# Optimization experiments

Measured on AMD Instinct MI355X. Metric: run time of the kernel, lower is better.

Reference implementation:

```python
import jax, jax.numpy as jnp
import numpy as np

N_HEAD = 12


def setup_inputs() -> dict:
    key = jax.random.key(0)
    ks = jax.random.split(key, 6)
    B, T, C = 8, 1024, 768
    x = jax.random.normal(ks[0], (B, T, C), dtype=jnp.float32)
    w_attn = jax.random.normal(ks[1], (C, 3 * C), dtype=jnp.float32) * 0.02
    b_attn = jnp.zeros((3 * C,), dtype=jnp.float32)
    w_proj = jax.random.normal(ks[2], (C, C), dtype=jnp.float32) * 0.02
    b_proj = jnp.zeros((C,), dtype=jnp.float32)
    rel_emb = jax.random.normal(ks[3], (2 * 1024 - 1, C // N_HEAD), dtype=jnp.float32) * 0.02
    return {"x": x, "w_attn": w_attn, "b_attn": b_attn,
            "w_proj": w_proj, "b_proj": b_proj, "rel_emb": rel_emb}


def reference(x, w_attn, b_attn, w_proj, b_proj, rel_emb):
    b, t, c = x.shape
    h = N_HEAD
    d = c // h
    scale = d ** -0.5
    # fused QKV projection
    qkv = x @ w_attn + b_attn                       # [b, t, 3c]
    q, k, v = jnp.split(qkv, 3, axis=-1)
    split_heads = lambda z: z.reshape(b, t, h, d).transpose(0, 2, 1, 3)  # [b,h,t,d]
    q, k, v = map(split_heads, (q, k, v))
    q = q * scale
    # content scores
    scores = jnp.einsum('bhid,bhjd->bhij', q, k)    # [b,h,t,t]
    # relative position bias: embed lookup + rel-shift (zero row prepended, last dropped)
    rel = rel_emb[:t]                               # [t, d]
    rel = jnp.concatenate([jnp.zeros_like(rel[:1]), rel], axis=0)[:-1]
    scores = scores + jnp.einsum('bhid,jd->bhij', q, rel)
    # causal mask
    causal = jnp.tril(jnp.ones((t, t), dtype=bool))
    scores = jnp.where(causal, scores, -jnp.inf)
    probs = jax.nn.softmax(scores, axis=-1)
    y = jnp.einsum('bhij,bhjd->bhid', probs, v)     # [b,h,t,d]
    y = y.transpose(0, 2, 1, 3).reshape(b, t, c)
    return y @ w_proj + b_proj
```

## Files before the change

### kernel.cpp

```cpp
#include <hip/hip_runtime.h>
#include <stdint.h>


typedef __attribute__((ext_vector_type(8))) short short8;
typedef __attribute__((ext_vector_type(4))) float f32x4;
typedef __attribute__((ext_vector_type(4))) unsigned short ushort4v;

#define DEV static __device__ __forceinline__

DEV float bf2f(unsigned short u) {
    union { unsigned int u; float f; } v; v.u = ((unsigned int)u) << 16; return v.f;
}
DEV unsigned short f2bf(float f) {
    union { float f; unsigned int u; } v; v.f = f;
    unsigned int u = v.u;
    return (unsigned short)((u + 0x7fffu + ((u >> 16) & 1u)) >> 16);
}

typedef const __attribute__((address_space(1))) void* gas_ptr;
typedef __attribute__((address_space(3))) void* las_ptr;
DEV void glds16(const void* g, void* l) {
    __builtin_amdgcn_global_load_lds((gas_ptr)g, (las_ptr)l, 16, 0, 0);
}

__global__ void detect_dtype(const unsigned int* __restrict__ w, int* __restrict__ flag) {
    __shared__ int cnt;
    if (threadIdx.x == 0) cnt = 0;
    __syncthreads();
    int c = 0;
    for (int i = threadIdx.x; i < 8192; i += 256) {
        unsigned int b1 = (w[i] >> 8) & 0x7F;
        c += (b1 >= 0x38 && b1 <= 0x3E) ? 1 : 0;
    }
    atomicAdd(&cnt, c);
    __syncthreads();
    if (threadIdx.x == 0) *flag = (cnt > 4096) ? 1 : 0;
}

__global__ __launch_bounds__(256) void cast_x(
    const void* __restrict__ x, unsigned short* __restrict__ xo,
    const int* __restrict__ flag)
{
    int i = (blockIdx.x * 256 + threadIdx.x) * 4;
    if (*flag) {
        *(ushort4v*)(xo + i) = *(const ushort4v*)((const unsigned short*)x + i);
    } else {
        f32x4 v = *(const f32x4*)((const float*)x + i);
        ushort4v o;
#pragma unroll
        for (int j = 0; j < 4; ++j) o[j] = f2bf(v[j]);
        *(ushort4v*)(xo + i) = o;
    }
}

__global__ __launch_bounds__(256) void cast_small(
    const void* __restrict__ rel, const void* __restrict__ ba, const void* __restrict__ bp,
    unsigned short* __restrict__ rel_o, unsigned short* __restrict__ ba_o,
    unsigned short* __restrict__ bp_o, const int* __restrict__ flag)
{
    int i = blockIdx.x * 256 + threadIdx.x;
    if (i >= 134080) return;
    int isbf = *flag;
    const void* src; unsigned short* dst; int off;
    if (i < 131008)      { src = rel; dst = rel_o; off = i; }
    else if (i < 133312) { src = ba;  dst = ba_o;  off = i - 131008; }
    else                 { src = bp;  dst = bp_o;  off = i - 133312; }
    dst[off] = isbf ? ((const unsigned short*)src)[off]
                    : f2bf(((const float*)src)[off]);
}

__global__ __launch_bounds__(256) void transpose_w(
    const void* __restrict__ in, unsigned short* __restrict__ out,
    int R, int C, const int* __restrict__ flag)
{
    __shared__ unsigned short tile[64][66];
    const int t = threadIdx.x;
    const int cb = blockIdx.x * 64;
    const int rb = blockIdx.y * 64;
    if (*flag) {
        const unsigned short* inp = (const unsigned short*)in;
        const int c8 = (t & 7) * 8;
        const int r = t >> 3;
#pragma unroll
        for (int p = 0; p < 2; ++p) {
            int rr = r + p * 32;
            short8 v = *(const short8*)(inp + (size_t)(rb + rr) * C + cb + c8);
#pragma unroll
            for (int i = 0; i < 8; ++i) tile[rr][c8 + i] = (unsigned short)v[i];
        }
    } else {
        const float* inp = (const float*)in;
        const int c4 = (t & 15) * 4;
        const int r = t >> 4;
#pragma unroll
        for (int p = 0; p < 4; ++p) {
            int rr = r + p * 16;
            f32x4 v = *(const f32x4*)(inp + (size_t)(rb + rr) * C + cb + c4);
#pragma unroll
            for (int i = 0; i < 4; ++i) tile[rr][c4 + i] = f2bf(v[i]);
        }
    }
    __syncthreads();
    {
        const int c8 = (t & 7) * 8;
        const int r = t >> 3;
#pragma unroll
        for (int p = 0; p < 2; ++p) {
            int oc = r + p * 32;
            short8 v;
#pragma unroll
            for (int i = 0; i < 8; ++i) v[i] = (short)tile[c8 + i][oc];
            *(short8*)(out + (size_t)(cb + oc) * R + rb + c8) = v;
        }
    }
}

#define GEMM_PROLOG(A_, Bt_)                                                     \
    __shared__ __align__(16) unsigned short Abuf[128 * 32];                      \
    __shared__ __align__(16) unsigned short Bbuf[128 * 32];                      \
    const int t = threadIdx.x;                                                   \
    const int wave = t >> 6, lane = t & 63;                                      \
    const int lo = lane & 15, hi = lane >> 4;                                    \
    const int wr = wave >> 1, wc = wave & 1;                                     \
    const int bm = blockIdx.x * 128;                                             \
    const int bn = blockIdx.y * 128;                                             \
    int L0 = t << 4, L1 = (t + 256) << 4;                                        \
    int S0 = L0 ^ (((L0 >> 7) & 3) << 4);                                        \
    int S1 = L1 ^ (((L1 >> 7) & 3) << 4);                                        \
    int r0 = S0 >> 6, o0 = (S0 & 63) >> 1;                                       \
    int r1 = S1 >> 6, o1 = (S1 & 63) >> 1;                                       \
    const unsigned short* Ab = (A_) + (size_t)bm * 768;                          \
    const unsigned short* Bb = (Bt_) + (size_t)bn * 768;                         \
    char* lA0 = (char*)Abuf + ((wave * 64) << 4);                                \
    char* lA1 = (char*)Abuf + ((256 + wave * 64) << 4);                          \
    char* lB0 = (char*)Bbuf + ((wave * 64) << 4);                                \
    char* lB1 = (char*)Bbuf + ((256 + wave * 64) << 4);                          \
    const char* ap[4]; const char* bp_[4];                                       \
    _Pragma("unroll")                                                            \
    for (int m = 0; m < 4; ++m) {                                                \
        int Pa = ((wr * 64 + m * 16 + lo) << 6) + (hi << 4);                     \
        ap[m] = (const char*)Abuf + (Pa ^ (((Pa >> 7) & 3) << 4));               \
        int Pb = ((wc * 64 + m * 16 + lo) << 6) + (hi << 4);                     \
        bp_[m] = (const char*)Bbuf + (Pb ^ (((Pb >> 7) & 3) << 4));              \
    }                                                                            \
    f32x4 acc[4][4];                                                             \
    _Pragma("unroll")                                                            \
    for (int m = 0; m < 4; ++m)                                                  \
        _Pragma("unroll")                                                        \
        for (int n = 0; n < 4; ++n) acc[m][n] = (f32x4){0.f, 0.f, 0.f, 0.f};     \
    for (int k0 = 0; k0 < 768; k0 += 32) {                                       \
        glds16(Ab + (size_t)r0 * 768 + k0 + o0, lA0);                            \
        glds16(Ab + (size_t)r1 * 768 + k0 + o1, lA1);                            \
        glds16(Bb + (size_t)r0 * 768 + k0 + o0, lB0);                            \
        glds16(Bb + (size_t)r1 * 768 + k0 + o1, lB1);                            \
        __syncthreads();                                                         \
        short8 af[4], bfv[4];                                                    \
        _Pragma("unroll")                                                        \
        for (int m = 0; m < 4; ++m) af[m] = *(const short8*)ap[m];               \
        _Pragma("unroll")                                                        \
        for (int n = 0; n < 4; ++n) bfv[n] = *(const short8*)bp_[n];             \
        _Pragma("unroll")                                                        \
        for (int m = 0; m < 4; ++m)                                              \
            _Pragma("unroll")                                                    \
            for (int n = 0; n < 4; ++n)                                          \
                acc[m][n] = __builtin_amdgcn_mfma_f32_16x16x32_bf16(             \
                    af[m], bfv[n], acc[m][n], 0, 0, 0);                          \
        __syncthreads();                                                         \
    }

__global__ __launch_bounds__(256) void gemm_qkv(
    const unsigned short* __restrict__ A,
    const unsigned short* __restrict__ Bt,
    const unsigned short* __restrict__ bias,
    const unsigned short* __restrict__ rel,
    unsigned short* __restrict__ q_ws,
    unsigned short* __restrict__ k_ws,
    unsigned short* __restrict__ v_ws)
{
    GEMM_PROLOG(A, Bt)
    const int gm0 = bm + wr * 64 + hi * 4;
#pragma unroll
    for (int m = 0; m < 4; ++m) {
        int gm = gm0 + m * 16;
        int b_ = gm >> 10;
        int tt = gm & 1023;
#pragma unroll
        for (int n = 0; n < 4; ++n) {
            int col = bn + wc * 64 + n * 16 + lo;
            float bs = bf2f(bias[col]);
            if (col < 768) {
                int h = col >> 6, d = col & 63;
                size_t base = (((size_t)b_ * 12 + h) * 1024 + tt) * 64 + d;
#pragma unroll
                for (int j = 0; j < 4; ++j)
                    q_ws[base + (size_t)j * 64] = f2bf((acc[m][n][j] + bs) * 0.125f);
            } else if (col < 1536) {
                int h = (col - 768) >> 6, d = col & 63;
                size_t base = (((size_t)b_ * 12 + h) * 1024 + tt) * 64 + d;
#pragma unroll
                for (int j = 0; j < 4; ++j) {
                    int trow = tt + j;
                    float rv = (trow > 0) ? bf2f(rel[(size_t)(trow - 1) * 64 + d]) : 0.f;
                    k_ws[base + (size_t)j * 64] = f2bf(acc[m][n][j] + bs + rv);
                }
            } else {
                int h = (col - 1536) >> 6, d = col & 63;
                size_t vb = (((size_t)b_ * 12 + h) * 64 + d) * 1024 + tt;
                ushort4v pk;
#pragma unroll
                for (int j = 0; j < 4; ++j) pk[j] = f2bf(acc[m][n][j] + bs);
                *(ushort4v*)(v_ws + vb) = pk;
            }
        }
    }
}

__global__ __launch_bounds__(256) void gemm_proj(
    const unsigned short* __restrict__ A,
    const unsigned short* __restrict__ Bt,
    const unsigned short* __restrict__ bias,
    const int* __restrict__ flag,
    void* __restrict__ outv)
{
    GEMM_PROLOG(A, Bt)
    const int isbf = *flag;
    const int gm0 = bm + wr * 64 + hi * 4;
#pragma unroll
    for (int m = 0; m < 4; ++m) {
        int gm = gm0 + m * 16;
#pragma unroll
        for (int n = 0; n < 4; ++n) {
            int col = bn + wc * 64 + n * 16 + lo;
            float bs = bf2f(bias[col]);
#pragma unroll
            for (int j = 0; j < 4; ++j) {
                float v = acc[m][n][j] + bs;
                if (isbf)
                    ((unsigned short*)outv)[(size_t)(gm + j) * 768 + col] = f2bf(v);
                else
                    ((float*)outv)[(size_t)(gm + j) * 768 + col] = v;
            }
        }
    }
}

__global__ __launch_bounds__(256) void attn_fused(
    const unsigned short* __restrict__ q_ws,
    const unsigned short* __restrict__ k_ws,
    const unsigned short* __restrict__ v_ws,
    unsigned short* __restrict__ att)
{
    __shared__ __align__(16) unsigned short Kbuf[2][64 * 64];
    __shared__ __align__(16) unsigned short Vbuf[2][64 * 64];
    __shared__ __align__(16) unsigned short Pbuf[4][16 * 64];
    const int t = threadIdx.x;
    const int wave = t >> 6, lane = t & 63;
    const int lo = lane & 15, hi = lane >> 4;
    const int gid = blockIdx.x;
    const int xcd = gid & 7;
    const int c = gid >> 3;
    const int bh = xcd * 12 + (c % 12);
    const int pairIdx = c / 12;
    const int b_ = bh / 12, h = bh % 12;
    const size_t base = (size_t)bh * (1024 * 64);
    const unsigned short* Kb = k_ws + base;
    const unsigned short* Vb = v_ws + base;

    int L0 = t << 4, L1 = (t + 256) << 4;
    int S0 = L0 ^ (((L0 >> 7) & 7) << 4);
    int S1 = L1 ^ (((L1 >> 7) & 7) << 4);
    int r0 = S0 >> 7, o0 = (S0 & 127) >> 1;
    int r1 = S1 >> 7, o1 = (S1 & 127) >> 1;
    const int lof0 = (wave * 64) << 4;
    const int lof1 = (256 + wave * 64) << 4;

    int koff[4][2];
#pragma unroll
    for (int nt = 0; nt < 4; ++nt)
#pragma unroll
        for (int kc = 0; kc < 2; ++kc) {
            int P = ((nt * 16 + lo) << 7) + (kc << 6) + (hi << 4);
            koff[nt][kc] = P ^ (((P >> 7) & 7) << 4);
        }
    int poffR[2];
#pragma unroll
    for (int kc = 0; kc < 2; ++kc) {
        int P = (lo << 7) + (kc << 6) + (hi << 4);
        poffR[kc] = P ^ (((P >> 7) & 7) << 4);
    }
    int poffW[4][4];
#pragma unroll
    for (int nt = 0; nt < 4; ++nt)
#pragma unroll
        for (int j = 0; j < 4; ++j) {
            int P = ((hi * 4 + j) << 7) + ((nt * 16 + lo) << 1);
            poffW[nt][j] = P ^ (((P >> 7) & 7) << 4);
        }
    char* pb = (char*)&Pbuf[wave][0];

#pragma unroll 1
    for (int sel = 0; sel < 2; ++sel) {
        const int qt = sel ? pairIdx : (15 - pairIdx);
        const int q0w = qt * 64 + wave * 16;

        short8 qf[2];
#pragma unroll
        for (int kc = 0; kc < 2; ++kc)
            qf[kc] = *(const short8*)(q_ws + base +
                (size_t)(q0w + lo) * 64 + kc * 32 + hi * 8);

        f32x4 o[4];
        float mrun[4], lrun[4];
#pragma unroll
        for (int nt = 0; nt < 4; ++nt) o[nt] = (f32x4){0.f, 0.f, 0.f, 0.f};
#pragma unroll
        for (int j = 0; j < 4; ++j) { mrun[j] = -1e30f; lrun[j] = 0.f; }

        if (sel) __syncthreads();
        glds16(Kb + (size_t)r0 * 64 + o0, (char*)Kbuf[0] + lof0);
        glds16(Kb + (size_t)r1 * 64 + o1, (char*)Kbuf[0] + lof1);
        glds16(Vb + (size_t)r0 * 1024 + o0, (char*)Vbuf[0] + lof0);
        glds16(Vb + (size_t)r1 * 1024 + o1, (char*)Vbuf[0] + lof1);

        int cur = 0;
        const int nkt = qt + 1;
        for (int kt = 0; kt < nkt; ++kt) {
            __syncthreads();
            if (kt + 1 < nkt) {
                const int kn = (kt + 1) * 64;
                glds16(Kb + (size_t)(kn + r0) * 64 + o0, (char*)Kbuf[cur ^ 1] + lof0);
                glds16(Kb + (size_t)(kn + r1) * 64 + o1, (char*)Kbuf[cur ^ 1] + lof1);
                glds16(Vb + (size_t)r0 * 1024 + kn + o0, (char*)Vbuf[cur ^ 1] + lof0);
                glds16(Vb + (size_t)r1 * 1024 + kn + o1, (char*)Vbuf[cur ^ 1] + lof1);
            }
            const int kv0 = kt * 64;
            const char* Kc = (const char*)Kbuf[cur];
            const char* Vc = (const char*)Vbuf[cur];

            short8 kf[4][2];
#pragma unroll
            for (int nt = 0; nt < 4; ++nt)
#pragma unroll
                for (int kc = 0; kc < 2; ++kc)
                    kf[nt][kc] = *(const short8*)(Kc + koff[nt][kc]);
            f32x4 sc[4];
            __builtin_amdgcn_s_setprio(1);
#pragma unroll
            for (int nt = 0; nt < 4; ++nt) {
                f32x4 z = (f32x4){0.f, 0.f, 0.f, 0.f};
                z = __builtin_amdgcn_mfma_f32_16x16x32_bf16(qf[0], kf[nt][0], z, 0, 0, 0);
                z = __builtin_amdgcn_mfma_f32_16x16x32_bf16(qf[1], kf[nt][1], z, 0, 0, 0);
                sc[nt] = z;
            }
            __builtin_amdgcn_s_setprio(0);
            if (kv0 + 63 > q0w) {
#pragma unroll
                for (int nt = 0; nt < 4; ++nt)
#pragma unroll
                    for (int j = 0; j < 4; ++j) {
                        int qr = q0w + hi * 4 + j;
                        int kc_ = kv0 + nt * 16 + lo;
                        if (kc_ > qr) sc[nt][j] = -1e30f;
                    }
            }
            float mx[4];
            int need = 0;
#pragma unroll
            for (int j = 0; j < 4; ++j) {
                float m0 = fmaxf(fmaxf(sc[0][j], sc[1][j]), fmaxf(sc[2][j], sc[3][j]));
                m0 = fmaxf(m0, __shfl_xor(m0, 1));
                m0 = fmaxf(m0, __shfl_xor(m0, 2));
                m0 = fmaxf(m0, __shfl_xor(m0, 4));
                m0 = fmaxf(m0, __shfl_xor(m0, 8));
                mx[j] = m0;
                need |= (m0 > mrun[j] + 8.f) ? 1 : 0;
            }
            if (__any(need)) {
#pragma unroll
                for (int j = 0; j < 4; ++j) {
                    float nm = fmaxf(mrun[j], mx[j]);
                    float corr = __expf(mrun[j] - nm);
                    mrun[j] = nm;
                    lrun[j] *= corr;
#pragma unroll
                    for (int nt = 0; nt < 4; ++nt) o[nt][j] *= corr;
                }
            }
#pragma unroll
            for (int j = 0; j < 4; ++j) {
                float rs = 0.f;
#pragma unroll
                for (int nt = 0; nt < 4; ++nt) {
                    float p = __expf(sc[nt][j] - mrun[j]);
                    sc[nt][j] = p;
                    rs += p;
                }
                rs += __shfl_xor(rs, 1);
                rs += __shfl_xor(rs, 2);
                rs += __shfl_xor(rs, 4);
                rs += __shfl_xor(rs, 8);
                lrun[j] += rs;
            }
            short8 vf[4][2];
#pragma unroll
            for (int nt = 0; nt < 4; ++nt)
#pragma unroll
                for (int kc2 = 0; kc2 < 2; ++kc2)
                    vf[nt][kc2] = *(const short8*)(Vc + koff[nt][kc2]);
#pragma unroll
            for (int nt = 0; nt < 4; ++nt)
#pragma unroll
                for (int j = 0; j < 4; ++j)
                    *(unsigned short*)(pb + poffW[nt][j]) = f2bf(sc[nt][j]);
#pragma unroll
            for (int kc2 = 0; kc2 < 2; ++kc2) {
                short8 pf = *(const short8*)(pb + poffR[kc2]);
                __builtin_amdgcn_s_setprio(1);
#pragma unroll
                for (int nt = 0; nt < 4; ++nt)
                    o[nt] = __builtin_amdgcn_mfma_f32_16x16x32_bf16(pf, vf[nt][kc2], o[nt], 0, 0, 0);
                __builtin_amdgcn_s_setprio(0);
            }
            cur ^= 1;
        }
#pragma unroll
        for (int j = 0; j < 4; ++j) {
            int tt = q0w + hi * 4 + j;
            float inv = 1.f / lrun[j];
#pragma unroll
            for (int nt = 0; nt < 4; ++nt)
                att[((size_t)(b_ * 1024 + tt)) * 768 + h * 64 + nt * 16 + lo] =
                    f2bf(o[nt][j] * inv);
        }
    }
}

extern "C" void kernel_launch(void* const* d_in, const int* in_sizes, int n_in,
                              void* d_out, int out_size, void* d_ws, size_t ws_size,
                              hipStream_t stream) {
    const void* x      = d_in[0];
    const void* w_attn = d_in[1];
    const void* b_attn = d_in[2];
    const void* w_proj = d_in[3];
    const void* b_proj = d_in[4];
    const void* rel    = d_in[5];
    char* ws = (char*)d_ws;
    int*            flag = (int*)(ws + 0);
    unsigned short* wTa  = (unsigned short*)(ws + 4096);
    unsigned short* wTp  = (unsigned short*)(ws + 3543040);
    unsigned short* x_bf = (unsigned short*)(ws + 4722688);
    unsigned short* relb = (unsigned short*)(ws + 17305600);
    unsigned short* bab  = (unsigned short*)(ws + 17567616);
    unsigned short* bpb  = (unsigned short*)(ws + 17572224);
    unsigned short* q_ws = (unsigned short*)(ws + 17573760);
    unsigned short* k_ws = (unsigned short*)(ws + 30156672);
    unsigned short* v_ws = (unsigned short*)(ws + 42739584);
    unsigned short* att  = x_bf;

    detect_dtype<<<1, 256, 0, stream>>>((const unsigned int*)w_attn, flag);
    cast_x<<<6144, 256, 0, stream>>>(x, x_bf, flag);
    cast_small<<<524, 256, 0, stream>>>(rel, b_attn, b_proj, relb, bab, bpb, flag);
    transpose_w<<<dim3(36, 12), 256, 0, stream>>>(w_attn, wTa, 768, 2304, flag);
    transpose_w<<<dim3(12, 12), 256, 0, stream>>>(w_proj, wTp, 768, 768, flag);
    gemm_qkv<<<dim3(64, 18), 256, 0, stream>>>(x_bf, wTa, bab, relb, q_ws, k_ws, v_ws);
    attn_fused<<<768, 256, 0, stream>>>(q_ws, k_ws, v_ws, att);
    gemm_proj<<<dim3(64, 6), 256, 0, stream>>>(att, wTp, bpb, flag, (void*)d_out);
}
```

Measured before the change: 241.0 us.

## Transpose QK MFMA so each lane owns one query row, use exp2 softmax

Swaps the MFMA operands for the score tile so each lane holds scores for a single query row. The row max and sum then need two cross-lane shuffles instead of four per row, and the running max and sum become scalars per lane. The log2(e) factor is folded into the Q scale so exp2 can replace expf, and the lazy-rescale threshold is raised. The P write layout into LDS is changed to match, and correction and normalisation factors are broadcast back to the output layout with shuffles.

```diff
diff --git a/kernel.cpp b/kernel.cpp
--- a/kernel.cpp
+++ b/kernel.cpp
@@ -179,6 +179,7 @@
 {
     GEMM_PROLOG(A, Bt)
     const int gm0 = bm + wr * 64 + hi * 4;
+    const float QSCALE = 0.125f * 1.44269504f;
 #pragma unroll
     for (int m = 0; m < 4; ++m) {
         int gm = gm0 + m * 16;
@@ -193,7 +194,7 @@
                 size_t base = (((size_t)b_ * 12 + h) * 1024 + tt) * 64 + d;
 #pragma unroll
                 for (int j = 0; j < 4; ++j)
-                    q_ws[base + (size_t)j * 64] = f2bf((acc[m][n][j] + bs) * 0.125f);
+                    q_ws[base + (size_t)j * 64] = f2bf((acc[m][n][j] + bs) * QSCALE);
             } else if (col < 1536) {
                 int h = (col - 768) >> 6, d = col & 63;
                 size_t base = (((size_t)b_ * 12 + h) * 1024 + tt) * 64 + d;
@@ -265,6 +266,7 @@
     const size_t base = (size_t)bh * (1024 * 64);
     const unsigned short* Kb = k_ws + base;
     const unsigned short* Vb = v_ws + base;
+    const float DEFER_THR = 11.5f;
 
     int L0 = t << 4, L1 = (t + 256) << 4;
     int S0 = L0 ^ (((L0 >> 7) & 7) << 4);
@@ -293,8 +295,8 @@
     for (int nt = 0; nt < 4; ++nt)
 #pragma unroll
         for (int j = 0; j < 4; ++j) {
-            int P = ((hi * 4 + j) << 7) + ((nt * 16 + lo) << 1);
-            poffW[nt][j] = P ^ (((P >> 7) & 7) << 4);
+            int P = (lo << 7) + ((nt * 16 + hi * 4 + j) << 1);
+            poffW[nt][j] = P ^ ((lo & 7) << 4);
         }
     char* pb = (char*)&Pbuf[wave][0];
 
@@ -302,6 +304,7 @@
     for (int sel = 0; sel < 2; ++sel) {
         const int qt = sel ? pairIdx : (15 - pairIdx);
         const int q0w = qt * 64 + wave * 16;
+        const int qrow = q0w + lo;
 
         short8 qf[2];
 #pragma unroll
@@ -310,11 +313,9 @@
                 (size_t)(q0w + lo) * 64 + kc * 32 + hi * 8);
 
         f32x4 o[4];
-        float mrun[4], lrun[4];
+        float mrun = -1e30f, lrun = 0.f;
 #pragma unroll
         for (int nt = 0; nt < 4; ++nt) o[nt] = (f32x4){0.f, 0.f, 0.f, 0.f};
-#pragma unroll
-        for (int j = 0; j < 4; ++j) { mrun[j] = -1e30f; lrun[j] = 0.f; }
 
         if (sel) __syncthreads();
         glds16(Kb + (size_t)r0 * 64 + o0, (char*)Kbuf[0] + lof0);
@@ -348,8 +349,8 @@
 #pragma unroll
             for (int nt = 0; nt < 4; ++nt) {
                 f32x4 z = (f32x4){0.f, 0.f, 0.f, 0.f};
-                z = __builtin_amdgcn_mfma_f32_16x16x32_bf16(qf[0], kf[nt][0], z, 0, 0, 0);
-                z = __builtin_amdgcn_mfma_f32_16x16x32_bf16(qf[1], kf[nt][1], z, 0, 0, 0);
+                z = __builtin_amdgcn_mfma_f32_16x16x32_bf16(kf[nt][0], qf[0], z, 0, 0, 0);
+                z = __builtin_amdgcn_mfma_f32_16x16x32_bf16(kf[nt][1], qf[1], z, 0, 0, 0);
                 sc[nt] = z;
             }
             __builtin_amdgcn_s_setprio(0);
@@ -358,49 +359,44 @@
                 for (int nt = 0; nt < 4; ++nt)
 #pragma unroll
                     for (int j = 0; j < 4; ++j) {
-                        int qr = q0w + hi * 4 + j;
-                        int kc_ = kv0 + nt * 16 + lo;
-                        if (kc_ > qr) sc[nt][j] = -1e30f;
+                        int kc_ = kv0 + nt * 16 + hi * 4 + j;
+                        if (kc_ > qrow) sc[nt][j] = -1e30f;
                     }
             }
-            float mx[4];
-            int need = 0;
-#pragma unroll
-            for (int j = 0; j < 4; ++j) {
-                float m0 = fmaxf(fmaxf(sc[0][j], sc[1][j]), fmaxf(sc[2][j], sc[3][j]));
-                m0 = fmaxf(m0, __shfl_xor(m0, 1));
-                m0 = fmaxf(m0, __shfl_xor(m0, 2));
-                m0 = fmaxf(m0, __shfl_xor(m0, 4));
-                m0 = fmaxf(m0, __shfl_xor(m0, 8));
-                mx[j] = m0;
-                need |= (m0 > mrun[j] + 8.f) ? 1 : 0;
-            }
-            if (__any(need)) {
+            float m0;
+            {
+                float a0 = fmaxf(fmaxf(sc[0][0], sc[0][1]), fmaxf(sc[0][2], sc[0][3]));
+                float a1 = fmaxf(fmaxf(sc[1][0], sc[1][1]), fmaxf(sc[1][2], sc[1][3]));
+                float a2 = fmaxf(fmaxf(sc[2][0], sc[2][1]), fmaxf(sc[2][2], sc[2][3]));
+                float a3 = fmaxf(fmaxf(sc[3][0], sc[3][1]), fmaxf(sc[3][2], sc[3][3]));
+                m0 = fmaxf(fmaxf(a0, a1), fmaxf(a2, a3));
+            }
+            m0 = fmaxf(m0, __shfl_xor(m0, 16));
+            m0 = fmaxf(m0, __shfl_xor(m0, 32));
+            if (__any(m0 > mrun + DEFER_THR)) {
+                float nm = fmaxf(mrun, m0);
+                float corr = __builtin_amdgcn_exp2f(mrun - nm);
+                mrun = nm;
+                lrun *= corr;
 #pragma unroll
                 for (int j = 0; j < 4; ++j) {
-                    float nm = fmaxf(mrun[j], mx[j]);
-                    float corr = __expf(mrun[j] - nm);
-                    mrun[j] = nm;
-                    lrun[j] *= corr;
-#pragma unroll
-                    for (int nt = 0; nt < 4; ++nt) o[nt][j] *= corr;
+                    float cj = __shfl(corr, hi * 4 + j);
+#pragma unroll
+                    for (int nt = 0; nt < 4; ++nt) o[nt][j] *= cj;
                 }
             }
-#pragma unroll
-            for (int j = 0; j < 4; ++j) {
-                float rs = 0.f;
-#pragma unroll
-                for (int nt = 0; nt < 4; ++nt) {
-                    float p = __expf(sc[nt][j] - mrun[j]);
+            float rs = 0.f;
+#pragma unroll
+            for (int nt = 0; nt < 4; ++nt)
+#pragma unroll
+                for (int j = 0; j < 4; ++j) {
+                    float p = __builtin_amdgcn_exp2f(sc[nt][j] - mrun);
                     sc[nt][j] = p;
                     rs += p;
                 }
-                rs += __shfl_xor(rs, 1);
-                rs += __shfl_xor(rs, 2);
-                rs += __shfl_xor(rs, 4);
-                rs += __shfl_xor(rs, 8);
-                lrun[j] += rs;
-            }
+            rs += __shfl_xor(rs, 16);
+            rs += __shfl_xor(rs, 32);
+            lrun += rs;
             short8 vf[4][2];
 #pragma unroll
             for (int nt = 0; nt < 4; ++nt)
@@ -425,8 +421,9 @@
         }
 #pragma unroll
         for (int j = 0; j < 4; ++j) {
+            float lj = __shfl(lrun, hi * 4 + j);
+            float inv = 1.f / lj;
             int tt = q0w + hi * 4 + j;
-            float inv = 1.f / lrun[j];
 #pragma unroll
             for (int nt = 0; nt < 4; ++nt)
                 att[((size_t)(b_ * 1024 + tt)) * 768 + h * 64 + nt * 16 + lo] =
```

Result: faster. 215.0 us (-10.8%).
